# Kernel optimization log

Hardware: AMD Instinct MI355X
Metric: run time of the kernel (lower is better)

Reference implementation:

```python
import jax, jax.numpy as jnp
import numpy as np

D_K = 128

def setup_inputs() -> dict:
    key = jax.random.key(0)
    k1, k2, k3 = jax.random.split(key, 3)
    q = jax.random.normal(k1, (8192, D_K), dtype=jnp.float32)
    k = jax.random.normal(k2, (8192, D_K), dtype=jnp.float32)
    v = jax.random.normal(k3, (8192, D_K), dtype=jnp.float32)
    return {"q": q, "k": k, "v": v}

def reference(q, k, v):
    # scores: [S_q, S_k]
    scores = jnp.einsum('qd,kd->qk', q, k) / jnp.sqrt(jnp.float32(D_K))
    attn = jax.nn.softmax(scores, axis=-1)  # softmax over keys (torch default last dim)
    return jnp.einsum('qk,kd->qd', attn, v)
```

## Files before the change

kernel.cpp:

```cpp
#include <hip/hip_runtime.h>
#include <math.h>


typedef _Float16 f16x8 __attribute__((ext_vector_type(8)));
typedef float    f32x16 __attribute__((ext_vector_type(16)));

constexpr int S_LEN = 8192;
constexpr int D_K   = 128;

constexpr size_t WS_L_OFF = 0;
constexpr size_t KV_OFF   = 524288;
constexpr size_t PART_OFF = KV_OFF + (size_t)256 * 16384;
constexpr size_t WS_NEED  = PART_OFF + (size_t)16 * S_LEN * 64 * 4;

#define CSCALE (0.08838834764831845f * 1.44269504088896340736f)

union UH8 { _Float16 h[8]; uint4 q; f16x8 v; };
union UF4 { unsigned u[4]; uint4 q; f16x8 v; };
union UHP { unsigned u; _Float16 h[2]; };

__device__ inline void async16(const uint4* g, uint4* l) {
  __builtin_amdgcn_global_load_lds(
      (const __attribute__((address_space(1))) unsigned int*)g,
      (__attribute__((address_space(3))) unsigned int*)l, 16, 0, 0);
}

template <bool ZOUT>
__global__ __launch_bounds__(512) void attn_prep(const float* __restrict__ K,
                                                 const float* __restrict__ V,
                                                 float* __restrict__ out,
                                                 char* __restrict__ ws) {
  const int t = blockIdx.x * 512 + threadIdx.x;
  uint4* KVg = (uint4*)(ws + KV_OFF);
  if (t < 131072) {
    int kt = t >> 9, idx = t & 511;
    int lane = idx & 63, s = idx >> 6;
    int key = kt * 32 + (lane & 31);
    int d0  = s * 16 + (lane >> 5) * 8;
    const float4* src = (const float4*)(K + (size_t)key * D_K + d0);
    float4 a = src[0], b = src[1];
    float f[8] = {a.x, a.y, a.z, a.w, b.x, b.y, b.z, b.w};
    UH8 h;
    #pragma unroll
    for (int j = 0; j < 8; ++j) h.h[j] = (_Float16)f[j];
    KVg[(size_t)kt * 1024 + idx] = h.q;
  } else if (t < 262144) {
    int g = t - 131072;
    int kt = g >> 9, idx = g & 511;
    int lane = idx & 63, c = (idx >> 6) & 3, kstep = idx >> 8;
    int d  = c * 32 + (lane & 31);
    int kb = kt * 32 + kstep * 16 + (lane >> 5) * 8;
    UH8 h;
    #pragma unroll
    for (int j = 0; j < 8; ++j) h.h[j] = (_Float16)V[(size_t)(kb + j) * D_K + d];
    KVg[(size_t)kt * 1024 + 512 + idx] = h.q;
  } else if (ZOUT && t < 327680) {
    int i = t - 262144;
    float4 z = make_float4(0.f, 0.f, 0.f, 0.f);
    float4* o4 = (float4*)out;
    #pragma unroll
    for (int j = 0; j < 4; ++j) o4[(size_t)i * 4 + j] = z;
  } else if (ZOUT && t < 329728) {
    int i = t - 327680;
    ((float4*)(ws + WS_L_OFF))[i] = make_float4(0.f, 0.f, 0.f, 0.f);
  }
}

template <bool PARTIAL>
__global__ __launch_bounds__(256, PARTIAL ? 4 : 2)
void attn_main(const float* __restrict__ Qg, float* __restrict__ out,
               char* __restrict__ ws) {
  constexpr int NSL   = PARTIAL ? 16 : 8;
  constexpr int ITERS = (S_LEN / NSL) / 32;

  __shared__ uint4 KV[2][1024];

  const int tid   = threadIdx.x;
  const int wave  = tid >> 6;
  const int lane  = tid & 63;
  const int lrow  = lane & 31;
  const int lhalf = lane >> 5;

  const int blk = blockIdx.x;
  const int ks  = blk & (NSL - 1);
  const int qb  = blk / NSL;
  const int qw  = qb * 128 + wave * 32;

  float* ws_l = (float*)(ws + WS_L_OFF);

  f16x8 qf[8];
  {
    const int q = qw + lrow;
    #pragma unroll
    for (int s = 0; s < 8; ++s) {
      const float4* src = (const float4*)(Qg + (size_t)q * D_K + s * 16 + lhalf * 8);
      float4 a = src[0], b = src[1];
      float f[8] = {a.x, a.y, a.z, a.w, b.x, b.y, b.z, b.w};
      UH8 h;
      #pragma unroll
      for (int j = 0; j < 8; ++j) h.h[j] = (_Float16)(f[j] * CSCALE);
      qf[s] = h.v;
    }
  }

  f32x16 O0{}, O1{}, O2{}, O3{};
  float lsum = 0.f;

  const uint4* KVg = (const uint4*)(ws + KV_OFF);

  {
    const size_t base = (size_t)(ks * ITERS) * 1024;
    #pragma unroll
    for (int i = 0; i < 4; ++i)
      async16(KVg + base + i * 256 + tid, &KV[0][i * 256 + tid]);
  }

  for (int it = 0; it < ITERS; ++it) {
    const int buf = it & 1;
    __syncthreads();

    if (it + 1 < ITERS) {
      const size_t base = (size_t)(ks * ITERS + it + 1) * 1024;
      #pragma unroll
      for (int i = 0; i < 4; ++i)
        async16(KVg + base + i * 256 + tid, &KV[buf ^ 1][i * 256 + tid]);
    }

    f32x16 Sa{}, Sb{};
    #pragma unroll
    for (int s = 0; s < 4; ++s) {
      f16x8 ka = __builtin_bit_cast(f16x8, KV[buf][(2 * s    ) * 64 + lane]);
      f16x8 kb = __builtin_bit_cast(f16x8, KV[buf][(2 * s + 1) * 64 + lane]);
      Sa = __builtin_amdgcn_mfma_f32_32x32x16_f16(ka, qf[2 * s    ], Sa, 0, 0, 0);
      Sb = __builtin_amdgcn_mfma_f32_32x32x16_f16(kb, qf[2 * s + 1], Sb, 0, 0, 0);
    }

    unsigned pk[8];
    #pragma unroll
    for (int i = 0; i < 8; ++i) {
      float p0 = __builtin_amdgcn_exp2f(Sa[2 * i]     + Sb[2 * i]);
      float p1 = __builtin_amdgcn_exp2f(Sa[2 * i + 1] + Sb[2 * i + 1]);
      lsum += p0 + p1;
      pk[i] = __builtin_bit_cast(unsigned, __builtin_amdgcn_cvt_pkrtz(p0, p1));
    }

    unsigned s0 = __shfl_xor(pk[0], 32), s1 = __shfl_xor(pk[1], 32);
    unsigned s2 = __shfl_xor(pk[2], 32), s3 = __shfl_xor(pk[3], 32);
    unsigned s4 = __shfl_xor(pk[4], 32), s5 = __shfl_xor(pk[5], 32);
    unsigned s6 = __shfl_xor(pk[6], 32), s7 = __shfl_xor(pk[7], 32);
    UF4 A0, A1;
    A0.u[0] = lhalf ? s2 : pk[0];
    A0.u[1] = lhalf ? s3 : pk[1];
    A0.u[2] = lhalf ? pk[2] : s0;
    A0.u[3] = lhalf ? pk[3] : s1;
    A1.u[0] = lhalf ? s6 : pk[4];
    A1.u[1] = lhalf ? s7 : pk[5];
    A1.u[2] = lhalf ? pk[6] : s4;
    A1.u[3] = lhalf ? pk[7] : s5;

    #pragma unroll
    for (int kstep = 0; kstep < 2; ++kstep) {
      f16x8 pf = kstep ? A1.v : A0.v;
      f16x8 v0 = __builtin_bit_cast(f16x8, KV[buf][512 + kstep * 256 +   0 + lane]);
      f16x8 v1 = __builtin_bit_cast(f16x8, KV[buf][512 + kstep * 256 +  64 + lane]);
      f16x8 v2 = __builtin_bit_cast(f16x8, KV[buf][512 + kstep * 256 + 128 + lane]);
      f16x8 v3 = __builtin_bit_cast(f16x8, KV[buf][512 + kstep * 256 + 192 + lane]);
      O0 = __builtin_amdgcn_mfma_f32_32x32x16_f16(pf, v0, O0, 0, 0, 0);
      O1 = __builtin_amdgcn_mfma_f32_32x32x16_f16(pf, v1, O1, 0, 0, 0);
      O2 = __builtin_amdgcn_mfma_f32_32x32x16_f16(pf, v2, O2, 0, 0, 0);
      O3 = __builtin_amdgcn_mfma_f32_32x32x16_f16(pf, v3, O3, 0, 0, 0);
    }
  }

  lsum += __shfl_xor(lsum, 32);

  if (PARTIAL) {
    if (lhalf == 0) ws_l[ks * S_LEN + qw + lrow] = lsum;
    unsigned* obase = (unsigned*)(ws + PART_OFF)
                    + (size_t)ks * S_LEN * 64 + (size_t)qw * 64;
    #pragma unroll
    for (int r = 0; r < 16; ++r) {
      int row = (r & 3) + 8 * (r >> 2) + 4 * lhalf;
      unsigned p02 = __builtin_bit_cast(unsigned, __builtin_amdgcn_cvt_pkrtz(O0[r], O2[r]));
      unsigned p13 = __builtin_bit_cast(unsigned, __builtin_amdgcn_cvt_pkrtz(O1[r], O3[r]));
      obase[(size_t)row * 64 + lrow]      = p02;
      obase[(size_t)row * 64 + 32 + lrow] = p13;
    }
  } else {
    if (lhalf == 0) atomicAdd(ws_l + qw + lrow, lsum);
    #pragma unroll
    for (int r = 0; r < 16; ++r) {
      int row = (r & 3) + 8 * (r >> 2) + 4 * lhalf;
      float* dst = out + (size_t)(qw + row) * D_K + lrow;
      atomicAdd(dst +  0, O0[r]);
      atomicAdd(dst + 32, O1[r]);
      atomicAdd(dst + 64, O2[r]);
      atomicAdd(dst + 96, O3[r]);
    }
  }
}

__global__ __launch_bounds__(256) void attn_norm16(float* __restrict__ out,
                                                   const float* __restrict__ lpart,
                                                   const unsigned* __restrict__ opart) {
  int t = blockIdx.x * 256 + threadIdx.x;
  int q  = t >> 4;
  int cg = t & 15;

  float l = 0.f;
  #pragma unroll
  for (int s = 0; s < 16; ++s) l += lpart[s * S_LEN + q];
  float inv = 1.0f / l;

  float acc[8] = {0.f, 0.f, 0.f, 0.f, 0.f, 0.f, 0.f, 0.f};
  #pragma unroll
  for (int s = 0; s < 16; ++s) {
    const uint4* src = (const uint4*)(opart + (size_t)s * S_LEN * 64
                                      + (size_t)q * 64 + 4 * cg);
    uint4 u = src[0];
    UHP a, b, c, d;
    a.u = u.x; b.u = u.y; c.u = u.z; d.u = u.w;
    acc[0] += (float)a.h[0]; acc[4] += (float)a.h[1];
    acc[1] += (float)b.h[0]; acc[5] += (float)b.h[1];
    acc[2] += (float)c.h[0]; acc[6] += (float)c.h[1];
    acc[3] += (float)d.h[0]; acc[7] += (float)d.h[1];
  }
  float4* o4 = (float4*)out;
  o4[(size_t)q * 32 + cg] =
      make_float4(acc[0] * inv, acc[1] * inv, acc[2] * inv, acc[3] * inv);
  o4[(size_t)q * 32 + 16 + cg] =
      make_float4(acc[4] * inv, acc[5] * inv, acc[6] * inv, acc[7] * inv);
}

__global__ __launch_bounds__(256) void attn_norm_fb(float* __restrict__ out,
                                                    const float* __restrict__ ws_l) {
  int i = blockIdx.x * 256 + threadIdx.x;
  float4* o4 = (float4*)out;
  float4 o = o4[i];
  float inv = 1.0f / ws_l[i >> 5];
  o.x *= inv; o.y *= inv; o.z *= inv; o.w *= inv;
  o4[i] = o;
}

extern "C" void kernel_launch(void* const* d_in, const int* in_sizes, int n_in,
                              void* d_out, int out_size, void* d_ws, size_t ws_size,
                              hipStream_t stream) {
  const float* q = (const float*)d_in[0];
  const float* k = (const float*)d_in[1];
  const float* v = (const float*)d_in[2];
  float* out = (float*)d_out;
  char* ws = (char*)d_ws;

  if (ws_size >= WS_NEED) {
    attn_prep<false><<<dim3(512), dim3(512), 0, stream>>>(k, v, out, ws);
    attn_main<true><<<dim3(1024), dim3(256), 0, stream>>>(q, out, ws);
    attn_norm16<<<dim3(512), dim3(256), 0, stream>>>(
        out, (const float*)(ws + WS_L_OFF), (const unsigned*)(ws + PART_OFF));
  } else {
    attn_prep<true><<<dim3(645), dim3(512), 0, stream>>>(k, v, out, ws);
    attn_main<false><<<dim3(512), dim3(256), 0, stream>>>(q, out, ws);
    attn_norm_fb<<<dim3(1024), dim3(256), 0, stream>>>(
        out, (const float*)(ws + WS_L_OFF));
  }
}
```

Baseline: 131.2 us.

## Process two 32-row query tiles per wave to reuse K/V LDS fragments

Each wave now handles 64 query rows (two 32-row tiles) instead of 32. Each K and V fragment read from LDS feeds two MFMAs, which halves LDS traffic and global K/V staging per query, and the grid is halved to match. The S computation now uses a single accumulator chain per tile over 8 steps instead of two chains over 4. The cost is roughly double the accumulator registers, so occupancy is capped at 2 blocks per CU and fewer blocks are in flight.

```diff
diff --git a/kernel.cpp b/kernel.cpp
--- a/kernel.cpp
+++ b/kernel.cpp
@@ -67,7 +67,7 @@
 }
 
 template <bool PARTIAL>
-__global__ __launch_bounds__(256, PARTIAL ? 4 : 2)
+__global__ __launch_bounds__(256, 2)
 void attn_main(const float* __restrict__ Qg, float* __restrict__ out,
                char* __restrict__ ws) {
   constexpr int NSL   = PARTIAL ? 16 : 8;
@@ -84,27 +84,34 @@
   const int blk = blockIdx.x;
   const int ks  = blk & (NSL - 1);
   const int qb  = blk / NSL;
-  const int qw  = qb * 128 + wave * 32;
+  const int qw  = qb * 256 + wave * 64;
 
   float* ws_l = (float*)(ws + WS_L_OFF);
 
-  f16x8 qf[8];
+  f16x8 qf0[8], qf1[8];
   {
-    const int q = qw + lrow;
     #pragma unroll
     for (int s = 0; s < 8; ++s) {
-      const float4* src = (const float4*)(Qg + (size_t)q * D_K + s * 16 + lhalf * 8);
-      float4 a = src[0], b = src[1];
-      float f[8] = {a.x, a.y, a.z, a.w, b.x, b.y, b.z, b.w};
-      UH8 h;
+      const int d0 = s * 16 + lhalf * 8;
+      const float4* s0 = (const float4*)(Qg + (size_t)(qw + lrow) * D_K + d0);
+      const float4* s1 = (const float4*)(Qg + (size_t)(qw + 32 + lrow) * D_K + d0);
+      float4 a0 = s0[0], b0 = s0[1], a1 = s1[0], b1 = s1[1];
+      float f0[8] = {a0.x, a0.y, a0.z, a0.w, b0.x, b0.y, b0.z, b0.w};
+      float f1[8] = {a1.x, a1.y, a1.z, a1.w, b1.x, b1.y, b1.z, b1.w};
+      UH8 h0, h1;
       #pragma unroll
-      for (int j = 0; j < 8; ++j) h.h[j] = (_Float16)(f[j] * CSCALE);
-      qf[s] = h.v;
-    }
-  }
-
-  f32x16 O0{}, O1{}, O2{}, O3{};
-  float lsum = 0.f;
+      for (int j = 0; j < 8; ++j) {
+        h0.h[j] = (_Float16)(f0[j] * CSCALE);
+        h1.h[j] = (_Float16)(f1[j] * CSCALE);
+      }
+      qf0[s] = h0.v;
+      qf1[s] = h1.v;
+    }
+  }
+
+  f32x16 O00{}, O01{}, O02{}, O03{};
+  f32x16 O10{}, O11{}, O12{}, O13{};
+  float lsum0 = 0.f, lsum1 = 0.f;
 
   const uint4* KVg = (const uint4*)(ws + KV_OFF);
 
@@ -126,76 +133,119 @@
         async16(KVg + base + i * 256 + tid, &KV[buf ^ 1][i * 256 + tid]);
     }
 
-    f32x16 Sa{}, Sb{};
-    #pragma unroll
-    for (int s = 0; s < 4; ++s) {
-      f16x8 ka = __builtin_bit_cast(f16x8, KV[buf][(2 * s    ) * 64 + lane]);
-      f16x8 kb = __builtin_bit_cast(f16x8, KV[buf][(2 * s + 1) * 64 + lane]);
-      Sa = __builtin_amdgcn_mfma_f32_32x32x16_f16(ka, qf[2 * s    ], Sa, 0, 0, 0);
-      Sb = __builtin_amdgcn_mfma_f32_32x32x16_f16(kb, qf[2 * s + 1], Sb, 0, 0, 0);
-    }
-
-    unsigned pk[8];
-    #pragma unroll
-    for (int i = 0; i < 8; ++i) {
-      float p0 = __builtin_amdgcn_exp2f(Sa[2 * i]     + Sb[2 * i]);
-      float p1 = __builtin_amdgcn_exp2f(Sa[2 * i + 1] + Sb[2 * i + 1]);
-      lsum += p0 + p1;
-      pk[i] = __builtin_bit_cast(unsigned, __builtin_amdgcn_cvt_pkrtz(p0, p1));
-    }
-
-    unsigned s0 = __shfl_xor(pk[0], 32), s1 = __shfl_xor(pk[1], 32);
-    unsigned s2 = __shfl_xor(pk[2], 32), s3 = __shfl_xor(pk[3], 32);
-    unsigned s4 = __shfl_xor(pk[4], 32), s5 = __shfl_xor(pk[5], 32);
-    unsigned s6 = __shfl_xor(pk[6], 32), s7 = __shfl_xor(pk[7], 32);
-    UF4 A0, A1;
-    A0.u[0] = lhalf ? s2 : pk[0];
-    A0.u[1] = lhalf ? s3 : pk[1];
-    A0.u[2] = lhalf ? pk[2] : s0;
-    A0.u[3] = lhalf ? pk[3] : s1;
-    A1.u[0] = lhalf ? s6 : pk[4];
-    A1.u[1] = lhalf ? s7 : pk[5];
-    A1.u[2] = lhalf ? pk[6] : s4;
-    A1.u[3] = lhalf ? pk[7] : s5;
+    f32x16 S0{}, S1{};
+    #pragma unroll
+    for (int s = 0; s < 8; ++s) {
+      f16x8 kf = __builtin_bit_cast(f16x8, KV[buf][s * 64 + lane]);
+      S0 = __builtin_amdgcn_mfma_f32_32x32x16_f16(kf, qf0[s], S0, 0, 0, 0);
+      S1 = __builtin_amdgcn_mfma_f32_32x32x16_f16(kf, qf1[s], S1, 0, 0, 0);
+    }
+
+    UF4 A00, A01, A10, A11;
+    {
+      unsigned pk[8];
+      #pragma unroll
+      for (int i = 0; i < 8; ++i) {
+        float p0 = __builtin_amdgcn_exp2f(S0[2 * i]);
+        float p1 = __builtin_amdgcn_exp2f(S0[2 * i + 1]);
+        lsum0 += p0 + p1;
+        pk[i] = __builtin_bit_cast(unsigned, __builtin_amdgcn_cvt_pkrtz(p0, p1));
+      }
+      unsigned s0 = __shfl_xor(pk[0], 32), s1 = __shfl_xor(pk[1], 32);
+      unsigned s2 = __shfl_xor(pk[2], 32), s3 = __shfl_xor(pk[3], 32);
+      unsigned s4 = __shfl_xor(pk[4], 32), s5 = __shfl_xor(pk[5], 32);
+      unsigned s6 = __shfl_xor(pk[6], 32), s7 = __shfl_xor(pk[7], 32);
+      A00.u[0] = lhalf ? s2 : pk[0];
+      A00.u[1] = lhalf ? s3 : pk[1];
+      A00.u[2] = lhalf ? pk[2] : s0;
+      A00.u[3] = lhalf ? pk[3] : s1;
+      A01.u[0] = lhalf ? s6 : pk[4];
+      A01.u[1] = lhalf ? s7 : pk[5];
+      A01.u[2] = lhalf ? pk[6] : s4;
+      A01.u[3] = lhalf ? pk[7] : s5;
+    }
+    {
+      unsigned pk[8];
+      #pragma unroll
+      for (int i = 0; i < 8; ++i) {
+        float p0 = __builtin_amdgcn_exp2f(S1[2 * i]);
+        float p1 = __builtin_amdgcn_exp2f(S1[2 * i + 1]);
+        lsum1 += p0 + p1;
+        pk[i] = __builtin_bit_cast(unsigned, __builtin_amdgcn_cvt_pkrtz(p0, p1));
+      }
+      unsigned s0 = __shfl_xor(pk[0], 32), s1 = __shfl_xor(pk[1], 32);
+      unsigned s2 = __shfl_xor(pk[2], 32), s3 = __shfl_xor(pk[3], 32);
+      unsigned s4 = __shfl_xor(pk[4], 32), s5 = __shfl_xor(pk[5], 32);
+      unsigned s6 = __shfl_xor(pk[6], 32), s7 = __shfl_xor(pk[7], 32);
+      A10.u[0] = lhalf ? s2 : pk[0];
+      A10.u[1] = lhalf ? s3 : pk[1];
+      A10.u[2] = lhalf ? pk[2] : s0;
+      A10.u[3] = lhalf ? pk[3] : s1;
+      A11.u[0] = lhalf ? s6 : pk[4];
+      A11.u[1] = lhalf ? s7 : pk[5];
+      A11.u[2] = lhalf ? pk[6] : s4;
+      A11.u[3] = lhalf ? pk[7] : s5;
+    }
 
     #pragma unroll
     for (int kstep = 0; kstep < 2; ++kstep) {
-      f16x8 pf = kstep ? A1.v : A0.v;
+      f16x8 p0 = kstep ? A01.v : A00.v;
+      f16x8 p1 = kstep ? A11.v : A10.v;
       f16x8 v0 = __builtin_bit_cast(f16x8, KV[buf][512 + kstep * 256 +   0 + lane]);
       f16x8 v1 = __builtin_bit_cast(f16x8, KV[buf][512 + kstep * 256 +  64 + lane]);
       f16x8 v2 = __builtin_bit_cast(f16x8, KV[buf][512 + kstep * 256 + 128 + lane]);
       f16x8 v3 = __builtin_bit_cast(f16x8, KV[buf][512 + kstep * 256 + 192 + lane]);
-      O0 = __builtin_amdgcn_mfma_f32_32x32x16_f16(pf, v0, O0, 0, 0, 0);
-      O1 = __builtin_amdgcn_mfma_f32_32x32x16_f16(pf, v1, O1, 0, 0, 0);
-      O2 = __builtin_amdgcn_mfma_f32_32x32x16_f16(pf, v2, O2, 0, 0, 0);
-      O3 = __builtin_amdgcn_mfma_f32_32x32x16_f16(pf, v3, O3, 0, 0, 0);
-    }
-  }
-
-  lsum += __shfl_xor(lsum, 32);
+      O00 = __builtin_amdgcn_mfma_f32_32x32x16_f16(p0, v0, O00, 0, 0, 0);
+      O10 = __builtin_amdgcn_mfma_f32_32x32x16_f16(p1, v0, O10, 0, 0, 0);
+      O01 = __builtin_amdgcn_mfma_f32_32x32x16_f16(p0, v1, O01, 0, 0, 0);
+      O11 = __builtin_amdgcn_mfma_f32_32x32x16_f16(p1, v1, O11, 0, 0, 0);
+      O02 = __builtin_amdgcn_mfma_f32_32x32x16_f16(p0, v2, O02, 0, 0, 0);
+      O12 = __builtin_amdgcn_mfma_f32_32x32x16_f16(p1, v2, O12, 0, 0, 0);
+      O03 = __builtin_amdgcn_mfma_f32_32x32x16_f16(p0, v3, O03, 0, 0, 0);
+      O13 = __builtin_amdgcn_mfma_f32_32x32x16_f16(p1, v3, O13, 0, 0, 0);
+    }
+  }
+
+  lsum0 += __shfl_xor(lsum0, 32);
+  lsum1 += __shfl_xor(lsum1, 32);
 
   if (PARTIAL) {
-    if (lhalf == 0) ws_l[ks * S_LEN + qw + lrow] = lsum;
-    unsigned* obase = (unsigned*)(ws + PART_OFF)
-                    + (size_t)ks * S_LEN * 64 + (size_t)qw * 64;
+    if (lhalf == 0) {
+      ws_l[ks * S_LEN + qw + lrow]      = lsum0;
+      ws_l[ks * S_LEN + qw + 32 + lrow] = lsum1;
+    }
+    unsigned* ob0 = (unsigned*)(ws + PART_OFF)
+                  + (size_t)ks * S_LEN * 64 + (size_t)qw * 64;
     #pragma unroll
     for (int r = 0; r < 16; ++r) {
       int row = (r & 3) + 8 * (r >> 2) + 4 * lhalf;
-      unsigned p02 = __builtin_bit_cast(unsigned, __builtin_amdgcn_cvt_pkrtz(O0[r], O2[r]));
-      unsigned p13 = __builtin_bit_cast(unsigned, __builtin_amdgcn_cvt_pkrtz(O1[r], O3[r]));
-      obase[(size_t)row * 64 + lrow]      = p02;
-      obase[(size_t)row * 64 + 32 + lrow] = p13;
+      unsigned a02 = __builtin_bit_cast(unsigned, __builtin_amdgcn_cvt_pkrtz(O00[r], O02[r]));
+      unsigned a13 = __builtin_bit_cast(unsigned, __builtin_amdgcn_cvt_pkrtz(O01[r], O03[r]));
+      unsigned b02 = __builtin_bit_cast(unsigned, __builtin_amdgcn_cvt_pkrtz(O10[r], O12[r]));
+      unsigned b13 = __builtin_bit_cast(unsigned, __builtin_amdgcn_cvt_pkrtz(O11[r], O13[r]));
+      ob0[(size_t)row * 64 + lrow]             = a02;
+      ob0[(size_t)row * 64 + 32 + lrow]        = a13;
+      ob0[(size_t)(row + 32) * 64 + lrow]      = b02;
+      ob0[(size_t)(row + 32) * 64 + 32 + lrow] = b13;
     }
   } else {
-    if (lhalf == 0) atomicAdd(ws_l + qw + lrow, lsum);
+    if (lhalf == 0) {
+      atomicAdd(ws_l + qw + lrow, lsum0);
+      atomicAdd(ws_l + qw + 32 + lrow, lsum1);
+    }
     #pragma unroll
     for (int r = 0; r < 16; ++r) {
       int row = (r & 3) + 8 * (r >> 2) + 4 * lhalf;
-      float* dst = out + (size_t)(qw + row) * D_K + lrow;
-      atomicAdd(dst +  0, O0[r]);
-      atomicAdd(dst + 32, O1[r]);
-      atomicAdd(dst + 64, O2[r]);
-      atomicAdd(dst + 96, O3[r]);
+      float* d0 = out + (size_t)(qw + row) * D_K + lrow;
+      atomicAdd(d0 +  0, O00[r]);
+      atomicAdd(d0 + 32, O01[r]);
+      atomicAdd(d0 + 64, O02[r]);
+      atomicAdd(d0 + 96, O03[r]);
+      float* d1 = out + (size_t)(qw + 32 + row) * D_K + lrow;
+      atomicAdd(d1 +  0, O10[r]);
+      atomicAdd(d1 + 32, O11[r]);
+      atomicAdd(d1 + 64, O12[r]);
+      atomicAdd(d1 + 96, O13[r]);
     }
   }
 }
@@ -253,12 +303,12 @@
 
   if (ws_size >= WS_NEED) {
     attn_prep<false><<<dim3(512), dim3(512), 0, stream>>>(k, v, out, ws);
-    attn_main<true><<<dim3(1024), dim3(256), 0, stream>>>(q, out, ws);
+    attn_main<true><<<dim3(512), dim3(256), 0, stream>>>(q, out, ws);
     attn_norm16<<<dim3(512), dim3(256), 0, stream>>>(
         out, (const float*)(ws + WS_L_OFF), (const unsigned*)(ws + PART_OFF));
   } else {
     attn_prep<true><<<dim3(645), dim3(512), 0, stream>>>(k, v, out, ws);
-    attn_main<false><<<dim3(512), dim3(256), 0, stream>>>(q, out, ws);
+    attn_main<false><<<dim3(256), dim3(256), 0, stream>>>(q, out, ws);
     attn_norm_fb<<<dim3(1024), dim3(256), 0, stream>>>(
         out, (const float*)(ws + WS_L_OFF));
   }
```

Result: faster. 116.7 us (-11.1%).
